# Kernel optimization log

Measured on AMD Instinct MI355X. Metric: run time of the kernel, lower is better.

## Reference

```python
import jax, jax.numpy as jnp
import numpy as np

# FP4 E2M1 representable magnitudes (sign handled separately)
_FP4_GRID = np.array([0.0, 0.5, 1.0, 1.5, 2.0, 3.0, 4.0, 6.0], dtype=np.float32)
_FP4_MIDS = (_FP4_GRID[:-1] + _FP4_GRID[1:]) / 2.0  # round-to-nearest boundaries


def fp4_quant_dequant(w):
    """Per-tensor absmax-scaled round-to-nearest FP4 (E2M1) fake quantization."""
    grid = jnp.asarray(_FP4_GRID, dtype=w.dtype)
    mids = jnp.asarray(_FP4_MIDS, dtype=w.dtype)
    scale = jnp.max(jnp.abs(w)) / 6.0  # map absmax -> top FP4 level
    a = jnp.abs(w) / scale
    idx = jnp.searchsorted(mids, a)  # nearest grid index via boundary search
    return grid[idx] * jnp.sign(w) * scale


def fp4_linear(x, W, b):
    # dequantized-weight matmul + bias, as in FP4Linear
    Wq = fp4_quant_dequant(W)
    return x @ Wq.T + b


def setup_inputs() -> dict:
    key = jax.random.key(0)
    k1, k2, k3, k4, k5 = jax.random.split(key, 5)
    B, D_IN, D_H, D_OUT = 8192, 2048, 8192, 2048
    x = jax.random.normal(k1, (B, D_IN), dtype=jnp.float32)
    W1 = jax.random.normal(k2, (D_H, D_IN), dtype=jnp.float32) * 0.02
    b1 = jax.random.normal(k3, (D_H,), dtype=jnp.float32) * 0.02
    W2 = jax.random.normal(k4, (D_OUT, D_H), dtype=jnp.float32) * 0.02
    b2 = jax.random.normal(k5, (D_OUT,), dtype=jnp.float32) * 0.02
    return {"x": x, "W1": W1, "b1": b1, "W2": W2, "b2": b2}


def reference(x, W1, b1, W2, b2):
    h = jax.nn.relu(fp4_linear(x, W1, b1))  # [B, hidden]
    y = fp4_linear(h, W2, b2)                # [B, out]
    return y
```

## Files before the change

kernel.cpp:

```cpp
#include <hip/hip_runtime.h>
#include <hip/hip_bf16.h>
#include <stdint.h>

typedef __attribute__((ext_vector_type(8))) short short8;
typedef __attribute__((ext_vector_type(4))) float f32x4;

#define AS1 __attribute__((address_space(1)))
#define AS3 __attribute__((address_space(3)))

static __device__ __forceinline__ unsigned short f2bf(float f) {
    unsigned int u = __float_as_uint(f);
    u += 0x7FFFu + ((u >> 16) & 1u);
    return (unsigned short)(u >> 16);
}

__global__ void init_amax(unsigned int* amax) {
    if (threadIdx.x < 2) amax[threadIdx.x] = 0u;
}

__global__ void absmax_kernel(const float4* __restrict__ w, size_t n4,
                              unsigned int* __restrict__ out) {
    float m = 0.0f;
    size_t i = (size_t)blockIdx.x * blockDim.x + threadIdx.x;
    size_t stride = (size_t)gridDim.x * blockDim.x;
    for (; i < n4; i += stride) {
        float4 v = w[i];
        m = fmaxf(m, fmaxf(fmaxf(fabsf(v.x), fabsf(v.y)),
                           fmaxf(fabsf(v.z), fabsf(v.w))));
    }
    #pragma unroll
    for (int off = 32; off > 0; off >>= 1)
        m = fmaxf(m, __shfl_down(m, off, 64));
    __shared__ float sm[4];
    int lane = threadIdx.x & 63, wid = threadIdx.x >> 6;
    if (lane == 0) sm[wid] = m;
    __syncthreads();
    if (threadIdx.x == 0) {
        float bm = fmaxf(fmaxf(sm[0], sm[1]), fmaxf(sm[2], sm[3]));
        atomicMax(out, __float_as_uint(bm));
    }
}

static __device__ __forceinline__ unsigned short quant_one(float wv, float scale) {
    float a = fabsf(wv) / scale;
    int idx = (a > 0.25f) + (a > 0.75f) + (a > 1.25f) + (a > 1.75f)
            + (a > 2.5f)  + (a > 3.5f)  + (a > 5.0f);
    const unsigned long long lo = 0x3FC03F803F000000ull;
    const unsigned long long hi = 0x40C0408040404000ull;
    unsigned long long tab = (idx < 4) ? lo : hi;
    unsigned short mag = (unsigned short)(tab >> ((idx & 3) * 16));
    unsigned short sgn = (unsigned short)((__float_as_uint(wv) >> 16) & 0x8000u);
    return (unsigned short)(mag | sgn);
}

__global__ void quant_kernel(const float4* __restrict__ w, size_t n4,
                             const unsigned int* __restrict__ amax,
                             ushort4* __restrict__ q) {
    const float scale = __uint_as_float(*amax) / 6.0f;
    size_t i = (size_t)blockIdx.x * blockDim.x + threadIdx.x;
    size_t stride = (size_t)gridDim.x * blockDim.x;
    for (; i < n4; i += stride) {
        float4 v = w[i];
        ushort4 o;
        o.x = quant_one(v.x, scale);
        o.y = quant_one(v.y, scale);
        o.z = quant_one(v.z, scale);
        o.w = quant_one(v.w, scale);
        q[i] = o;
    }
}

__global__ void cast_bf16_kernel(const float4* __restrict__ x, size_t n4,
                                 ushort4* __restrict__ o) {
    size_t i = (size_t)blockIdx.x * blockDim.x + threadIdx.x;
    size_t stride = (size_t)gridDim.x * blockDim.x;
    for (; i < n4; i += stride) {
        float4 v = x[i];
        ushort4 r;
        r.x = f2bf(v.x); r.y = f2bf(v.y); r.z = f2bf(v.z); r.w = f2bf(v.w);
        o[i] = r;
    }
}


#define GLL(gp, dst)                                                    \
    __builtin_amdgcn_global_load_lds((const AS1 unsigned int*)(gp),     \
        (AS3 unsigned int*)(dst), 16, 0, 0)

#define STAGE(bufw, sA, sB)                                             \
    do {                                                                \
        GLL(pA + (sA) + goffA0, lds + (bufw) + tid * 16);               \
        GLL(pA + (sA) + goffA1, lds + (bufw) + 4096 + tid * 16);        \
        GLL(pA + (sA) + goffA2, lds + (bufw) + 8192 + tid * 16);        \
        GLL(pA + (sA) + goffA3, lds + (bufw) + 12288 + tid * 16);       \
        GLL(pB + (sB) + goffB0, lds + (bufw) + 16384 + tid * 16);       \
        GLL(pB + (sB) + goffB1, lds + (bufw) + 20480 + tid * 16);       \
    } while (0)

#define RD_B(bufr)                                                      \
    do {                                                                \
        _Pragma("unroll") for (int _j = 0; _j < 4; ++_j)                \
            b_[_j] = *(const short8*)(ldsB + (bufr) + _j * 1024);       \
    } while (0)

#define RD_A(bufr)                                                      \
    do {                                                                \
        _Pragma("unroll") for (int _i = 0; _i < 8; ++_i)                \
            a_[_i] = *(const short8*)(ldsA + (bufr) + _i * 1024);       \
    } while (0)

#define MF4(I0)                                                                \
    do {                                                                       \
        _Pragma("unroll") for (int _i = 0; _i < 4; ++_i)                       \
            _Pragma("unroll") for (int _j = 0; _j < 4; ++_j)                   \
                acc[(I0) + _i][_j] = __builtin_amdgcn_mfma_f32_16x16x32_bf16(  \
                    a_[(I0) + _i], b_[_j], acc[(I0) + _i][_j], 0, 0, 0);       \
    } while (0)

#define BAR()  __builtin_amdgcn_s_barrier()
#define SCHB() __builtin_amdgcn_sched_barrier(0)
#define LGKM(n) do { SCHB(); asm volatile("s_waitcnt lgkmcnt(" #n ")"); SCHB(); } while (0)

template <int RELU_BF16, int LAYA>
__global__ __launch_bounds__(256, 2)
void gemmT(const char* __restrict__ A,
           const unsigned short* __restrict__ B,
           const float* __restrict__ bias,
           const unsigned int* __restrict__ amax,
           float* __restrict__ outF,
           char* __restrict__ outH,
           int N, int K, int gx, int cw, int NK) {
    __shared__ __align__(16) char lds[49152];

    const int tid  = threadIdx.x;
    const int lane = tid & 63;
    const int wid  = tid >> 6;
    const int wm   = wid >> 1;
    const int wn   = wid & 1;

    const int nwg = gridDim.x;
    const int wg  = blockIdx.x;
    const int c   = wg & 7;
    const int idx = wg >> 3;
    const int nc  = nwg >> 3;
    const int cxc = gx / cw;
    const int ox  = (c % cxc) * cw;
    const int oy  = (c / cxc) * (nc / cw);
    const int bx  = ox + idx % cw;
    const int by  = oy + idx / cw;
    const int col0 = bx * 128;
    const int row0 = by * 256;

    int sp = ((lane & 15) << 6) + ((lane >> 4) << 4);
    sp ^= ((sp >> 9) & 1) << 5;
    const char* ldsA = lds + wm * 8192 + sp;
    const char* ldsB = lds + 16384 + wn * 4096 + sp;

    int goffA0, goffA1, goffA2, goffA3, goffB0, goffB1;
    {
        #pragma unroll
        for (int j = 0; j < 4; ++j) {
            int o = j * 4096 + tid * 16;
            int st = o >> 10, b = o & 1023;
            b ^= ((b >> 9) & 1) << 5;
            int row = (st << 4) + (b >> 6);
            int k   = (b & 63) >> 1;
            int g = LAYA ? ((row >> 4) * 262144 + (k >> 4) * 512 +
                            (row & 3) * 128 + ((row >> 2) & 3) * 32 + (k & 15) * 2)
                         : (row * K + k) * 2;
            if (j == 0) goffA0 = g; else if (j == 1) goffA1 = g;
            else if (j == 2) goffA2 = g; else goffA3 = g;
        }
        #pragma unroll
        for (int j = 0; j < 2; ++j) {
            int o = j * 4096 + tid * 16;
            int st = o >> 10, b = o & 1023;
            b ^= ((b >> 9) & 1) << 5;
            int col = (st << 4) + (b >> 6);
            int k   = (b & 63) >> 1;
            int g = (col * K + k) * 2;
            if (j == 0) goffB0 = g; else goffB1 = g;
        }
    }
    const char* pA = A + (LAYA ? (size_t)(row0 >> 4) * 262144 : (size_t)row0 * K * 2);
    const char* pB = (const char*)B + (size_t)col0 * K * 2;
    const size_t dA = LAYA ? 1024 : 64;

    STAGE(0, 0, 0);
    asm volatile("s_waitcnt vmcnt(0)");
    BAR();

    f32x4 acc[8][4] = {};
    short8 a_[8], b_[4];

    for (int s = 0; s < NK - 1; ++s) {
        const int bufr = (s & 1) * 24576;
        const int bufw = bufr ^ 24576;
        STAGE(bufw, (size_t)(s + 1) * dA, (size_t)(s + 1) * 64);
        RD_B(bufr); RD_A(bufr);
        LGKM(4);
        MF4(0);
        LGKM(0);
        MF4(4);
        asm volatile("s_waitcnt vmcnt(0)");
        BAR();
    }
    {
        const int bufr = ((NK - 1) & 1) * 24576;
        RD_B(bufr); RD_A(bufr);
        LGKM(4);
        MF4(0);
        LGKM(0);
        MF4(4);
        BAR();
    }

    const float scale = __uint_as_float(*amax) / 6.0f;

    if (RELU_BF16) {
        const int gbit = (lane >> 4) * 32 + (lane & 15) * 2;
        #pragma unroll
        for (int j = 0; j < 4; ++j) {
            const int col = col0 + wn * 64 + j * 16 + (lane & 15);
            const float bvv = bias[col];
            const size_t ktb = (size_t)(((col0 + wn * 64) >> 4) + j) * 512;
            #pragma unroll
            for (int i = 0; i < 8; ++i) {
                const size_t rtb = (size_t)(((row0 + wm * 128) >> 4) + i) * 262144;
                #pragma unroll
                for (int r = 0; r < 4; ++r) {
                    float v = fmaxf(acc[i][j][r] * scale + bvv, 0.0f);
                    *(unsigned short*)(outH + rtb + ktb + r * 128 + gbit) = f2bf(v);
                }
            }
        }
    } else {
        #pragma unroll
        for (int p = 0; p < 4; ++p) {
            if (wm == (p >> 1)) {
                const int h = p & 1;
                #pragma unroll
                for (int j = 0; j < 4; ++j) {
                    const int colb = wn * 64 + j * 16 + (lane & 15);
                    const float bvv = bias[col0 + colb];
                    #pragma unroll
                    for (int ii = 0; ii < 4; ++ii) {
                        const int i = h * 4 + ii;
                        #pragma unroll
                        for (int r = 0; r < 4; ++r) {
                            const int row_l = ii * 16 + (lane >> 4) * 4 + r;
                            const int blk = (colb >> 2) ^ (((row_l >> 2) & 3) << 2);
                            *(float*)(lds + row_l * 512 + blk * 16 + (colb & 3) * 4)
                                = acc[i][j][r] * scale + bvv;
                        }
                    }
                }
            }
            asm volatile("s_waitcnt lgkmcnt(0)");
            BAR();
            #pragma unroll
            for (int q = 0; q < 8; ++q) {
                const int flat  = q * 4096 + tid * 16;
                const int row_l = flat >> 9;
                const int blk0  = (flat >> 4) & 31;
                const int blk   = blk0 ^ (((row_l >> 2) & 3) << 2);
                f32x4 v = *(const f32x4*)(lds + row_l * 512 + blk * 16);
                *(f32x4*)(outF + (size_t)(row0 + p * 64 + row_l) * N
                                 + col0 + blk0 * 4) = v;
            }
            BAR();
        }
    }
}

extern "C" void kernel_launch(void* const* d_in, const int* in_sizes, int n_in,
                              void* d_out, int out_size, void* d_ws, size_t ws_size,
                              hipStream_t stream) {
    const float* x  = (const float*)d_in[0];
    const float* W1 = (const float*)d_in[1];
    const float* b1 = (const float*)d_in[2];
    const float* W2 = (const float*)d_in[3];
    const float* b2 = (const float*)d_in[4];
    float* out = (float*)d_out;

    const int Bm = 8192, Din = 2048, Dh = 8192, Dout = 2048;
    const size_t nW1 = (size_t)Dh * Din;
    const size_t nW2 = (size_t)Dout * Dh;
    const size_t nX  = (size_t)Bm * Din;
    const size_t nH  = (size_t)Bm * Dh;

    const size_t need = 256 + 2 * (nW1 + nW2 + nX + nH);
    if (ws_size < need) return;

    uint8_t* ws = (uint8_t*)d_ws;
    unsigned int*   amax = (unsigned int*)ws;
    unsigned short* Q1 = (unsigned short*)(ws + 256);
    unsigned short* Q2 = Q1 + nW1;
    unsigned short* Xb = Q2 + nW2;
    char*           H  = (char*)(Xb + nX);

    init_amax<<<1, 64, 0, stream>>>(amax);
    absmax_kernel<<<1024, 256, 0, stream>>>((const float4*)W1, nW1 / 4, amax + 0);
    absmax_kernel<<<1024, 256, 0, stream>>>((const float4*)W2, nW2 / 4, amax + 1);
    quant_kernel<<<2048, 256, 0, stream>>>((const float4*)W1, nW1 / 4, amax + 0, (ushort4*)Q1);
    quant_kernel<<<2048, 256, 0, stream>>>((const float4*)W2, nW2 / 4, amax + 1, (ushort4*)Q2);
    cast_bf16_kernel<<<2048, 256, 0, stream>>>((const float4*)x, nX / 4, (ushort4*)Xb);

    gemmT<1, 0><<<dim3(2048), 256, 0, stream>>>(
        (const char*)Xb, Q1, b1, amax + 0, nullptr, H,
        Dh, Din, Dh / 128, 16, Din / 32);
    gemmT<0, 1><<<dim3(512), 256, 0, stream>>>(
        H, Q2, b2, amax + 1, out, nullptr,
        Dout, Dh, Dout / 128, 16, Dh / 32);
}
```

Measured before the change: 565.1 us.

## Enlarge GEMM tile to 256x256 with 8 waves and triple-buffered LDS pipeline

Reworks both GEMMs to use 256x256 output tiles per 512-thread workgroup, with three LDS buffers so global-to-LDS loads run two K-steps ahead. MFMA groups are wrapped in s_setprio to favour math issue. The goal is more operand reuse per loaded byte and better hiding of load latency. In exchange LDS use doubles to 96KB, the grid is smaller, and the epilogue staging stride changes, which may reduce occupancy and tail balance.

New measurement: 560.3 us. Within noise of the previous version (-0.8%).

```diff
diff --git a/kernel.cpp b/kernel.cpp
--- a/kernel.cpp
+++ b/kernel.cpp
@@ -87,56 +87,55 @@
     __builtin_amdgcn_global_load_lds((const AS1 unsigned int*)(gp),     \
         (AS3 unsigned int*)(dst), 16, 0, 0)
 
-#define STAGE(bufw, sA, sB)                                             \
-    do {                                                                \
-        GLL(pA + (sA) + goffA0, lds + (bufw) + tid * 16);               \
-        GLL(pA + (sA) + goffA1, lds + (bufw) + 4096 + tid * 16);        \
-        GLL(pA + (sA) + goffA2, lds + (bufw) + 8192 + tid * 16);        \
-        GLL(pA + (sA) + goffA3, lds + (bufw) + 12288 + tid * 16);       \
-        GLL(pB + (sB) + goffB0, lds + (bufw) + 16384 + tid * 16);       \
-        GLL(pB + (sB) + goffB1, lds + (bufw) + 20480 + tid * 16);       \
-    } while (0)
-
-#define RD_B(bufr)                                                      \
+#define STAGE_T(kt, bufw)                                                     \
+    do {                                                                      \
+        GLL(pA0 + (size_t)(kt) * dA + goffA, lds + (bufw) + tid * 16);        \
+        GLL(pA1 + (size_t)(kt) * dA + goffA, lds + (bufw) + 8192 + tid * 16); \
+        GLL(pB0 + (size_t)(kt) * 64 + goffB, lds + (bufw) + 16384 + tid * 16);\
+        GLL(pB1 + (size_t)(kt) * 64 + goffB, lds + (bufw) + 24576 + tid * 16);\
+    } while (0)
+
+#define RDB(bo)                                                         \
     do {                                                                \
         _Pragma("unroll") for (int _j = 0; _j < 4; ++_j)                \
-            b_[_j] = *(const short8*)(ldsB + (bufr) + _j * 1024);       \
-    } while (0)
-
-#define RD_A(bufr)                                                      \
+            b_[_j] = *(const short8*)(ldsB + (bo) + _j * 1024);         \
+    } while (0)
+
+#define RDA(bo, dst, s0)                                                \
     do {                                                                \
-        _Pragma("unroll") for (int _i = 0; _i < 8; ++_i)                \
-            a_[_i] = *(const short8*)(ldsA + (bufr) + _i * 1024);       \
-    } while (0)
-
-#define MF4(I0)                                                                \
+        _Pragma("unroll") for (int _i = 0; _i < 4; ++_i)                \
+            dst[_i] = *(const short8*)(ldsA + (bo) + ((s0) + _i) * 1024);\
+    } while (0)
+
+#define MFG16(I0, ARR)                                                         \
     do {                                                                       \
         _Pragma("unroll") for (int _i = 0; _i < 4; ++_i)                       \
             _Pragma("unroll") for (int _j = 0; _j < 4; ++_j)                   \
                 acc[(I0) + _i][_j] = __builtin_amdgcn_mfma_f32_16x16x32_bf16(  \
-                    a_[(I0) + _i], b_[_j], acc[(I0) + _i][_j], 0, 0, 0);       \
+                    ARR[_i], b_[_j], acc[(I0) + _i][_j], 0, 0, 0);             \
     } while (0)
 
 #define BAR()  __builtin_amdgcn_s_barrier()
+#define PRIO(x) __builtin_amdgcn_s_setprio(x)
 #define SCHB() __builtin_amdgcn_sched_barrier(0)
 #define LGKM(n) do { SCHB(); asm volatile("s_waitcnt lgkmcnt(" #n ")"); SCHB(); } while (0)
 
 template <int RELU_BF16, int LAYA>
-__global__ __launch_bounds__(256, 2)
-void gemmT(const char* __restrict__ A,
+__global__ __launch_bounds__(512, 2)
+void gemm3(const char* __restrict__ A,
            const unsigned short* __restrict__ B,
            const float* __restrict__ bias,
            const unsigned int* __restrict__ amax,
            float* __restrict__ outF,
            char* __restrict__ outH,
-           int N, int K, int gx, int cw, int NK) {
-    __shared__ __align__(16) char lds[49152];
+           int N, int K, int gx, int cw, int NT) {
+    __shared__ __align__(16) char lds[98304];
 
     const int tid  = threadIdx.x;
     const int lane = tid & 63;
     const int wid  = tid >> 6;
-    const int wm   = wid >> 1;
-    const int wn   = wid & 1;
+    const int wm   = wid >> 2;
+    const int wn   = wid & 3;
 
     const int nwg = gridDim.x;
     const int wg  = blockIdx.x;
@@ -148,71 +147,55 @@
     const int oy  = (c / cxc) * (nc / cw);
     const int bx  = ox + idx % cw;
     const int by  = oy + idx / cw;
-    const int col0 = bx * 128;
+    const int col0 = bx * 256;
     const int row0 = by * 256;
 
     int sp = ((lane & 15) << 6) + ((lane >> 4) << 4);
     sp ^= ((sp >> 9) & 1) << 5;
     const char* ldsA = lds + wm * 8192 + sp;
-    const char* ldsB = lds + 16384 + wn * 4096 + sp;
-
-    int goffA0, goffA1, goffA2, goffA3, goffB0, goffB1;
+    const char* ldsB = lds + 16384 + (wn >> 1) * 8192 + (wn & 1) * 4096 + sp;
+
+    int goffA, goffB;
     {
-        #pragma unroll
-        for (int j = 0; j < 4; ++j) {
-            int o = j * 4096 + tid * 16;
-            int st = o >> 10, b = o & 1023;
-            b ^= ((b >> 9) & 1) << 5;
-            int row = (st << 4) + (b >> 6);
-            int k   = (b & 63) >> 1;
-            int g = LAYA ? ((row >> 4) * 262144 + (k >> 4) * 512 +
-                            (row & 3) * 128 + ((row >> 2) & 3) * 32 + (k & 15) * 2)
-                         : (row * K + k) * 2;
-            if (j == 0) goffA0 = g; else if (j == 1) goffA1 = g;
-            else if (j == 2) goffA2 = g; else goffA3 = g;
-        }
-        #pragma unroll
-        for (int j = 0; j < 2; ++j) {
-            int o = j * 4096 + tid * 16;
-            int st = o >> 10, b = o & 1023;
-            b ^= ((b >> 9) & 1) << 5;
-            int col = (st << 4) + (b >> 6);
-            int k   = (b & 63) >> 1;
-            int g = (col * K + k) * 2;
-            if (j == 0) goffB0 = g; else goffB1 = g;
-        }
-    }
-    const char* pA = A + (LAYA ? (size_t)(row0 >> 4) * 262144 : (size_t)row0 * K * 2);
-    const char* pB = (const char*)B + (size_t)col0 * K * 2;
+        int o = tid * 16;
+        int s = o >> 10, b = o & 1023;
+        b ^= ((b >> 9) & 1) << 5;
+        int row = (s << 4) + (b >> 6);
+        int k   = (b & 63) >> 1;
+        goffA = LAYA ? ((row >> 4) * 262144 + (k >> 4) * 512 +
+                        (row & 3) * 128 + ((row >> 2) & 3) * 32 + (k & 15) * 2)
+                     : (row * K + k) * 2;
+        goffB = (row * K + k) * 2;
+    }
+    const char* pA0 = A + (LAYA ? (size_t)row0 * 16384 : (size_t)row0 * K * 2);
+    const char* pA1 = A + (LAYA ? (size_t)(row0 + 128) * 16384
+                                : (size_t)(row0 + 128) * K * 2);
+    const char* pB0 = (const char*)B + (size_t)col0 * K * 2;
+    const char* pB1 = (const char*)B + (size_t)(col0 + 128) * K * 2;
     const size_t dA = LAYA ? 1024 : 64;
 
-    STAGE(0, 0, 0);
-    asm volatile("s_waitcnt vmcnt(0)");
+    STAGE_T(0, 0);
+    STAGE_T(1, 32768);
+    asm volatile("s_waitcnt vmcnt(4)");
     BAR();
 
     f32x4 acc[8][4] = {};
-    short8 a_[8], b_[4];
-
-    for (int s = 0; s < NK - 1; ++s) {
-        const int bufr = (s & 1) * 24576;
-        const int bufw = bufr ^ 24576;
-        STAGE(bufw, (size_t)(s + 1) * dA, (size_t)(s + 1) * 64);
-        RD_B(bufr); RD_A(bufr);
+    short8 aP[4], aQ[4], b_[4];
+    int oc = 0, on = 32768, o2 = 65536;
+
+    for (int t = 0; t < NT; ++t) {
+        if (t + 2 < NT) STAGE_T(t + 2, o2);
+        RDB(oc);
+        RDA(oc, aP, 0);
+        RDA(oc, aQ, 4);
         LGKM(4);
-        MF4(0);
+        PRIO(1); MFG16(0, aP); PRIO(0);
         LGKM(0);
-        MF4(4);
-        asm volatile("s_waitcnt vmcnt(0)");
+        PRIO(1); MFG16(4, aQ); PRIO(0);
+        if (t + 2 < NT)      { asm volatile("s_waitcnt vmcnt(4)"); }
+        else if (t + 1 < NT) { asm volatile("s_waitcnt vmcnt(0)"); }
         BAR();
-    }
-    {
-        const int bufr = ((NK - 1) & 1) * 24576;
-        RD_B(bufr); RD_A(bufr);
-        LGKM(4);
-        MF4(0);
-        LGKM(0);
-        MF4(4);
-        BAR();
+        int tmp = oc; oc = on; on = o2; o2 = tmp;
     }
 
     const float scale = __uint_as_float(*amax) / 6.0f;
@@ -250,7 +233,7 @@
                         for (int r = 0; r < 4; ++r) {
                             const int row_l = ii * 16 + (lane >> 4) * 4 + r;
                             const int blk = (colb >> 2) ^ (((row_l >> 2) & 3) << 2);
-                            *(float*)(lds + row_l * 512 + blk * 16 + (colb & 3) * 4)
+                            *(float*)(lds + row_l * 1024 + blk * 16 + (colb & 3) * 4)
                                 = acc[i][j][r] * scale + bvv;
                         }
                     }
@@ -260,11 +243,11 @@
             BAR();
             #pragma unroll
             for (int q = 0; q < 8; ++q) {
-                const int flat  = q * 4096 + tid * 16;
-                const int row_l = flat >> 9;
-                const int blk0  = (flat >> 4) & 31;
+                const int flat  = q * 8192 + tid * 16;
+                const int row_l = flat >> 10;
+                const int blk0  = (flat >> 4) & 63;
                 const int blk   = blk0 ^ (((row_l >> 2) & 3) << 2);
-                f32x4 v = *(const f32x4*)(lds + row_l * 512 + blk * 16);
+                f32x4 v = *(const f32x4*)(lds + row_l * 1024 + blk * 16);
                 *(f32x4*)(outF + (size_t)(row0 + p * 64 + row_l) * N
                                  + col0 + blk0 * 4) = v;
             }
@@ -306,10 +289,10 @@
     quant_kernel<<<2048, 256, 0, stream>>>((const float4*)W2, nW2 / 4, amax + 1, (ushort4*)Q2);
     cast_bf16_kernel<<<2048, 256, 0, stream>>>((const float4*)x, nX / 4, (ushort4*)Xb);
 
-    gemmT<1, 0><<<dim3(2048), 256, 0, stream>>>(
+    gemm3<1, 0><<<dim3((Dh / 256) * (Bm / 256)), 512, 0, stream>>>(
         (const char*)Xb, Q1, b1, amax + 0, nullptr, H,
-        Dh, Din, Dh / 128, 16, Din / 32);
-    gemmT<0, 1><<<dim3(512), 256, 0, stream>>>(
+        Dh, Din, Dh / 256, 16, Din / 32);
+    gemm3<0, 1><<<dim3((Dout / 256) * (Bm / 256)), 512, 0, stream>>>(
         H, Q2, b2, amax + 1, out, nullptr,
-        Dout, Dh, Dout / 128, 16, Dh / 32);
-}
+        Dout, Dh, Dout / 256, 8, Dh / 32);
+}
```
